# Kernel optimization log

Hardware: AMD Instinct MI355X
Metric: run time of the kernel (lower is better)

## Reference

```python
import jax, jax.numpy as jnp
import numpy as np

N_NODES, N_EDGES = 20000, 400000
IN_DIM, HC, OUT_DIM, EDGE_DIM = 128, 128, 128, 2


def _add_self_loops(src, dst, ea, n):
    # PyG fill_value='mean': self-loop edge_attr = mean of incoming edge_attr
    deg = jax.ops.segment_sum(jnp.ones(src.shape[0], ea.dtype), dst, num_segments=n)
    mean_ea = jax.ops.segment_sum(ea, dst, num_segments=n) / jnp.clip(deg, 1.0)[:, None]
    loop = jnp.arange(n, dtype=src.dtype)
    return (jnp.concatenate([src, loop]), jnp.concatenate([dst, loop]),
            jnp.concatenate([ea, mean_ea], axis=0))


def _gat(x, src, dst, ea, W, att_s, att_d, We, att_e, b, heads, out_ch, concat):
    n = x.shape[0]
    xh = (x @ W).reshape(n, heads, out_ch)                      # [N,H,C]
    a_src = jnp.einsum('nhc,hc->nh', xh, att_s)                  # [N,H]
    a_dst = jnp.einsum('nhc,hc->nh', xh, att_d)
    eh = (ea @ We).reshape(-1, heads, out_ch)                    # [E,H,C]
    a_e = jnp.einsum('ehc,hc->eh', eh, att_e)                    # [E,H]
    alpha = jax.nn.leaky_relu(a_src[src] + a_dst[dst] + a_e, 0.2)
    # segment softmax over destination nodes (every node has a self loop)
    amax = jax.ops.segment_max(alpha, dst, num_segments=n)
    amax = jnp.where(jnp.isfinite(amax), amax, 0.0)
    ex = jnp.exp(alpha - amax[dst])
    denom = jax.ops.segment_sum(ex, dst, num_segments=n)
    w = ex / (denom[dst] + 1e-16)                                # [E,H]
    out = jax.ops.segment_sum(xh[src] * w[..., None], dst, num_segments=n)  # [N,H,C]
    out = out.reshape(n, heads * out_ch) if concat else out.mean(axis=1)
    return out + b


def setup_inputs() -> dict:
    key = jax.random.key(0)
    ks = jax.random.split(key, 16)
    g = lambda k, shape, fan: jax.random.normal(k, shape, jnp.float32) * (1.0 / np.sqrt(fan))
    inp = {
        'x': jax.random.normal(ks[0], (N_NODES, IN_DIM), jnp.float32),
        'edge_index': jax.random.randint(ks[1], (2, N_EDGES), 0, N_NODES, jnp.int32),
        'edge_attr': jax.random.normal(ks[2], (N_EDGES, EDGE_DIM), jnp.float32),
        # conv1: GATConv(128 -> hc=128, heads=2, edge_dim=2, concat=True)
        'W1': g(ks[3], (IN_DIM, 2 * HC), IN_DIM),
        'att_s1': g(ks[4], (2, HC), HC),
        'att_d1': g(ks[5], (2, HC), HC),
        'We1': g(ks[6], (EDGE_DIM, 2 * HC), EDGE_DIM),
        'att_e1': g(ks[7], (2, HC), HC),
        'b1': jnp.zeros((2 * HC,), jnp.float32),
        # conv2: GATConv(256 -> 128, heads=1, edge_dim=2, concat=False)
        'W2': g(ks[8], (2 * HC, OUT_DIM), 2 * HC),
        'att_s2': g(ks[9], (1, OUT_DIM), OUT_DIM),
        'att_d2': g(ks[10], (1, OUT_DIM), OUT_DIM),
        'We2': g(ks[11], (EDGE_DIM, OUT_DIM), EDGE_DIM),
        'att_e2': g(ks[12], (1, OUT_DIM), OUT_DIM),
        'b2': jnp.zeros((OUT_DIM,), jnp.float32),
    }
    return inp


def reference(x, edge_index, edge_attr, W1, att_s1, att_d1, We1, att_e1, b1,
              W2, att_s2, att_d2, We2, att_e2, b2):
    n = x.shape[0]
    src0, dst0 = edge_index[0], edge_index[1]
    src, dst, ea = _add_self_loops(src0, dst0, edge_attr, n)
    x0 = x
    h = jax.nn.relu(_gat(x, src, dst, ea, W1, att_s1, att_d1, We1, att_e1, b1,
                         heads=2, out_ch=HC, concat=True))
    h = _gat(h, src, dst, ea, W2, att_s2, att_d2, We2, att_e2, b2,
             heads=1, out_ch=OUT_DIM, concat=False)
    # SimpleConv(aggr='mean'): mean over incoming neighbors on the ORIGINAL edges
    deg = jax.ops.segment_sum(jnp.ones(src0.shape[0], h.dtype), dst0, num_segments=n)
    mean_h = jax.ops.segment_sum(h[src0], dst0, num_segments=n) / jnp.clip(deg, 1.0)[:, None]
    return jax.nn.relu(mean_h + x0)
```

## Files before the change

kernel.cpp:

```cpp
#include <hip/hip_runtime.h>
#include <hip/hip_bf16.h>

#define NN 20000
#define NE 400000
#define SLOTS 64

typedef unsigned short u16;
typedef unsigned int u32;
typedef unsigned long long u64;

typedef __attribute__((ext_vector_type(8))) short bf16x8;
typedef __attribute__((ext_vector_type(4))) float f32x4;

__device__ __forceinline__ float bf2f(u16 u) {
    union { u32 i; float f; } v; v.i = ((u32)u) << 16; return v.f;
}
__device__ __forceinline__ u16 f2bf(float f) {
    __hip_bfloat16 h = __float2bfloat16(f);
    return *reinterpret_cast<u16*>(&h);
}
__device__ __forceinline__ u32 pack2(float lo, float hi) {
    return (u32)f2bf(lo) | ((u32)f2bf(hi) << 16);
}

__global__ void k_pre(const float* __restrict__ We1, const float* __restrict__ att_e1,
                      const float* __restrict__ We2, const float* __restrict__ att_e2,
                      const float* __restrict__ W1, const float* __restrict__ W2,
                      int* __restrict__ cnt, float* __restrict__ consts,
                      u16* __restrict__ Bt1, u16* __restrict__ Bt2) {
    int idx = blockIdx.x * 256 + threadIdx.x;
    if (idx < NN) cnt[idx] = 0;
    if (idx < 32768) {
        int n = idx >> 7, k = idx & 127;
        Bt1[idx] = f2bf(W1[k * 256 + n]);
    } else {
        int j = idx - 32768;
        int n = j >> 8, k = j & 255;
        Bt2[j] = f2bf(W2[k * 128 + n]);
    }
    if (blockIdx.x == 0) {
        __shared__ float red[128];
        int c = threadIdx.x;
        float p[6];
        if (c < 128) {
            p[0] = We1[0 * 256 + 0 * 128 + c] * att_e1[0 * 128 + c];
            p[1] = We1[0 * 256 + 1 * 128 + c] * att_e1[1 * 128 + c];
            p[2] = We1[1 * 256 + 0 * 128 + c] * att_e1[0 * 128 + c];
            p[3] = We1[1 * 256 + 1 * 128 + c] * att_e1[1 * 128 + c];
            p[4] = We2[0 * 128 + c] * att_e2[c];
            p[5] = We2[1 * 128 + c] * att_e2[c];
        }
        for (int j = 0; j < 6; j++) {
            if (c < 128) red[c] = p[j];
            __syncthreads();
            for (int off = 64; off >= 1; off >>= 1) {
                if (c < off) red[c] += red[c + off];
                __syncthreads();
            }
            if (c == 0) consts[j] = red[0];
            __syncthreads();
        }
    }
}

__global__ void k_build(const int* __restrict__ ei, const float* __restrict__ ea,
                        const float* __restrict__ consts, int* __restrict__ cnt,
                        float4* __restrict__ slot) {
    int e = blockIdx.x * 256 + threadIdx.x;
    if (e >= NE) return;
    int d = ei[NE + e];
    int s = ei[e];
    float2 v = *reinterpret_cast<const float2*>(ea + (size_t)e * 2);
    int pos = atomicAdd(&cnt[d], 1);
    if (pos < SLOTS) {
        float4 rec;
        rec.x = __int_as_float(s);
        rec.y = v.x * consts[0] + v.y * consts[2];
        rec.z = v.x * consts[1] + v.y * consts[3];
        rec.w = v.x * consts[4] + v.y * consts[5];
        slot[d * SLOTS + pos] = rec;
    }
}

__global__ __launch_bounds__(256) void k_gemm1(const float* __restrict__ A,
                                               const u16* __restrict__ Bt,
                                               const float* __restrict__ att_s,
                                               const float* __restrict__ att_d,
                                               u16* __restrict__ C,
                                               float2* __restrict__ a_s,
                                               float2* __restrict__ a_d) {
    constexpr int K = 128, KC = 4, NT = 16;
    int lane = threadIdx.x & 63;
    int wave = threadIdx.x >> 6;
    int r0 = (blockIdx.x * 4 + wave) * 16;
    if (r0 >= NN) return;
    int mrow = lane & 15, g = lane >> 4;
    int arow = r0 + mrow; if (arow >= NN) arow = NN - 1;
    const float* abase = A + (size_t)arow * K + g * 8;
    bf16x8 a[KC];
#pragma unroll
    for (int kc = 0; kc < KC; kc++) {
        float4 lo = *reinterpret_cast<const float4*>(abase + kc * 32);
        float4 hi = *reinterpret_cast<const float4*>(abase + kc * 32 + 4);
        bf16x8 t;
        t[0] = (short)f2bf(lo.x); t[1] = (short)f2bf(lo.y);
        t[2] = (short)f2bf(lo.z); t[3] = (short)f2bf(lo.w);
        t[4] = (short)f2bf(hi.x); t[5] = (short)f2bf(hi.y);
        t[6] = (short)f2bf(hi.z); t[7] = (short)f2bf(hi.w);
        a[kc] = t;
    }
    f32x4 acc[NT];
#pragma unroll
    for (int nt = 0; nt < NT; nt++) acc[nt] = (f32x4){0.f, 0.f, 0.f, 0.f};
#pragma unroll
    for (int nt = 0; nt < NT; nt++) {
        const u16* bbase = Bt + (size_t)(nt * 16 + mrow) * K + g * 8;
#pragma unroll
        for (int kc = 0; kc < KC; kc++) {
            bf16x8 b = *reinterpret_cast<const bf16x8*>(bbase + kc * 32);
            acc[nt] = __builtin_amdgcn_mfma_f32_16x16x32_bf16(a[kc], b, acc[nt], 0, 0, 0);
        }
    }
    int orow0 = r0 + g * 4;
#pragma unroll
    for (int nt = 0; nt < NT; nt++)
#pragma unroll
        for (int r = 0; r < 4; r++) {
            int rr = orow0 + r;
            if (rr < NN) C[(size_t)rr * 256 + nt * 16 + mrow] = f2bf(acc[nt][r]);
        }
    float attsv[NT], attdv[NT];
#pragma unroll
    for (int nt = 0; nt < NT; nt++) {
        attsv[nt] = att_s[nt * 16 + mrow];
        attdv[nt] = att_d[nt * 16 + mrow];
    }
#pragma unroll
    for (int r = 0; r < 4; r++) {
        float s0 = 0.f, s1 = 0.f, d0 = 0.f, d1 = 0.f;
#pragma unroll
        for (int nt = 0; nt < 8; nt++) { s0 += acc[nt][r] * attsv[nt]; d0 += acc[nt][r] * attdv[nt]; }
#pragma unroll
        for (int nt = 8; nt < NT; nt++) { s1 += acc[nt][r] * attsv[nt]; d1 += acc[nt][r] * attdv[nt]; }
        for (int off = 8; off >= 1; off >>= 1) {
            s0 += __shfl_xor(s0, off); s1 += __shfl_xor(s1, off);
            d0 += __shfl_xor(d0, off); d1 += __shfl_xor(d1, off);
        }
        int rr = orow0 + r;
        if (mrow == 0 && rr < NN) {
            a_s[rr] = make_float2(s0, s1);
            a_d[rr] = make_float2(d0, d1);
        }
    }
}

__global__ __launch_bounds__(256) void k_gemm2(const u16* __restrict__ A,
                                               const u16* __restrict__ Bt,
                                               const float* __restrict__ att_s,
                                               const float* __restrict__ att_d,
                                               u16* __restrict__ C,
                                               float* __restrict__ a_s,
                                               float* __restrict__ a_d) {
    constexpr int K = 256, KC = 8, NT = 8;
    int lane = threadIdx.x & 63;
    int wave = threadIdx.x >> 6;
    int r0 = (blockIdx.x * 4 + wave) * 16;
    if (r0 >= NN) return;
    int mrow = lane & 15, g = lane >> 4;
    int arow = r0 + mrow; if (arow >= NN) arow = NN - 1;
    const u16* abase = A + (size_t)arow * K + g * 8;
    bf16x8 a[KC];
#pragma unroll
    for (int kc = 0; kc < KC; kc++) a[kc] = *reinterpret_cast<const bf16x8*>(abase + kc * 32);
    f32x4 acc[NT];
#pragma unroll
    for (int nt = 0; nt < NT; nt++) acc[nt] = (f32x4){0.f, 0.f, 0.f, 0.f};
#pragma unroll
    for (int nt = 0; nt < NT; nt++) {
        const u16* bbase = Bt + (size_t)(nt * 16 + mrow) * K + g * 8;
#pragma unroll
        for (int kc = 0; kc < KC; kc++) {
            bf16x8 b = *reinterpret_cast<const bf16x8*>(bbase + kc * 32);
            acc[nt] = __builtin_amdgcn_mfma_f32_16x16x32_bf16(a[kc], b, acc[nt], 0, 0, 0);
        }
    }
    int orow0 = r0 + g * 4;
#pragma unroll
    for (int nt = 0; nt < NT; nt++)
#pragma unroll
        for (int r = 0; r < 4; r++) {
            int rr = orow0 + r;
            if (rr < NN) C[(size_t)rr * 128 + nt * 16 + mrow] = f2bf(acc[nt][r]);
        }
    float attsv[NT], attdv[NT];
#pragma unroll
    for (int nt = 0; nt < NT; nt++) {
        attsv[nt] = att_s[nt * 16 + mrow];
        attdv[nt] = att_d[nt * 16 + mrow];
    }
#pragma unroll
    for (int r = 0; r < 4; r++) {
        float s0 = 0.f, d0 = 0.f;
#pragma unroll
        for (int nt = 0; nt < NT; nt++) { s0 += acc[nt][r] * attsv[nt]; d0 += acc[nt][r] * attdv[nt]; }
        for (int off = 8; off >= 1; off >>= 1) {
            s0 += __shfl_xor(s0, off);
            d0 += __shfl_xor(d0, off);
        }
        int rr = orow0 + r;
        if (mrow == 0 && rr < NN) { a_s[rr] = s0; a_d[rr] = d0; }
    }
}

__global__ __launch_bounds__(256) void k_conv1(const int* __restrict__ cnt,
                                               const float4* __restrict__ slot,
                                               const u16* __restrict__ xh1,
                                               const float2* __restrict__ a_s,
                                               const float2* __restrict__ a_d,
                                               const float* __restrict__ b1,
                                               u16* __restrict__ h1out) {
    int lane = threadIdx.x & 63;
    int n = blockIdx.x * 4 + (threadIdx.x >> 6);
    if (n >= NN) return;
    int deg = cnt[n]; if (deg > SLOTS) deg = SLOTS;
    float2 ad = a_d[n];
    float2 asn = a_s[n];
    bool valid = lane < deg;
    int s = 0; float ae0 = 0.f, ae1 = 0.f;
    if (valid) {
        float4 rec = slot[n * SLOTS + lane];
        s = __float_as_int(rec.x);
        ae0 = rec.y; ae1 = rec.z;
    }
    float sum0 = ae0, sum1 = ae1;
    for (int off = 32; off >= 1; off >>= 1) {
        sum0 += __shfl_xor(sum0, off);
        sum1 += __shfl_xor(sum1, off);
    }
    float invdeg = 1.f / (float)(deg < 1 ? 1 : deg);
    float sae0 = sum0 * invdeg, sae1 = sum1 * invdeg;
    float2 asv = valid ? a_s[s] : make_float2(0.f, 0.f);
    float l0 = asv.x + ad.x + ae0;
    float l1 = asv.y + ad.y + ae1;
    l0 = l0 >= 0.f ? l0 : 0.2f * l0;
    l1 = l1 >= 0.f ? l1 : 0.2f * l1;
    if (!valid) { l0 = -3.4e38f; l1 = -3.4e38f; }
    float sl0 = asn.x + ad.x + sae0;
    float sl1 = asn.y + ad.y + sae1;
    sl0 = sl0 >= 0.f ? sl0 : 0.2f * sl0;
    sl1 = sl1 >= 0.f ? sl1 : 0.2f * sl1;
    float cm0 = l0, cm1 = l1;
    for (int off = 32; off >= 1; off >>= 1) {
        cm0 = fmaxf(cm0, __shfl_xor(cm0, off));
        cm1 = fmaxf(cm1, __shfl_xor(cm1, off));
    }
    float m0 = fmaxf(cm0, sl0), m1 = fmaxf(cm1, sl1);
    float e0 = valid ? __expf(l0 - m0) : 0.f;
    float e1 = valid ? __expf(l1 - m1) : 0.f;
    float es0 = __expf(sl0 - m0), es1 = __expf(sl1 - m1);
    float cs0 = e0, cs1 = e1;
    for (int off = 32; off >= 1; off >>= 1) {
        cs0 += __shfl_xor(cs0, off);
        cs1 += __shfl_xor(cs1, off);
    }
    float den0 = cs0 + es0 + 1e-16f, den1 = cs1 + es1 + 1e-16f;
    int q = lane >> 4, ql = lane & 15;
    int ch = ql * 16;
    int myh = ql >> 3;
    float acc[16];
#pragma unroll
    for (int i = 0; i < 16; i++) acc[i] = 0.f;
    for (int j = 0; j < deg; j += 4) {
        int jj = j + q;
        bool ve = jj < deg;
        int sj = ve ? __shfl(s, jj) : n;
        float w0 = __shfl(e0, jj), w1 = __shfl(e1, jj);
        float wj = ve ? (myh ? w1 : w0) : 0.f;
        const u16* p = xh1 + (size_t)sj * 256 + ch;
        uint4 va = *reinterpret_cast<const uint4*>(p);
        uint4 vb = *reinterpret_cast<const uint4*>(p + 8);
        acc[0] += wj * bf2f((u16)(va.x & 0xffff)); acc[1] += wj * bf2f((u16)(va.x >> 16));
        acc[2] += wj * bf2f((u16)(va.y & 0xffff)); acc[3] += wj * bf2f((u16)(va.y >> 16));
        acc[4] += wj * bf2f((u16)(va.z & 0xffff)); acc[5] += wj * bf2f((u16)(va.z >> 16));
        acc[6] += wj * bf2f((u16)(va.w & 0xffff)); acc[7] += wj * bf2f((u16)(va.w >> 16));
        acc[8] += wj * bf2f((u16)(vb.x & 0xffff)); acc[9] += wj * bf2f((u16)(vb.x >> 16));
        acc[10] += wj * bf2f((u16)(vb.y & 0xffff)); acc[11] += wj * bf2f((u16)(vb.y >> 16));
        acc[12] += wj * bf2f((u16)(vb.z & 0xffff)); acc[13] += wj * bf2f((u16)(vb.z >> 16));
        acc[14] += wj * bf2f((u16)(vb.w & 0xffff)); acc[15] += wj * bf2f((u16)(vb.w >> 16));
    }
#pragma unroll
    for (int i = 0; i < 16; i++) {
        acc[i] += __shfl_xor(acc[i], 16);
        acc[i] += __shfl_xor(acc[i], 32);
    }
    if (q == 0) {
        float ws = myh ? es1 : es0;
        const u16* p = xh1 + (size_t)n * 256 + ch;
        uint4 va = *reinterpret_cast<const uint4*>(p);
        uint4 vb = *reinterpret_cast<const uint4*>(p + 8);
        acc[0] += ws * bf2f((u16)(va.x & 0xffff)); acc[1] += ws * bf2f((u16)(va.x >> 16));
        acc[2] += ws * bf2f((u16)(va.y & 0xffff)); acc[3] += ws * bf2f((u16)(va.y >> 16));
        acc[4] += ws * bf2f((u16)(va.z & 0xffff)); acc[5] += ws * bf2f((u16)(va.z >> 16));
        acc[6] += ws * bf2f((u16)(va.w & 0xffff)); acc[7] += ws * bf2f((u16)(va.w >> 16));
        acc[8] += ws * bf2f((u16)(vb.x & 0xffff)); acc[9] += ws * bf2f((u16)(vb.x >> 16));
        acc[10] += ws * bf2f((u16)(vb.y & 0xffff)); acc[11] += ws * bf2f((u16)(vb.y >> 16));
        acc[12] += ws * bf2f((u16)(vb.z & 0xffff)); acc[13] += ws * bf2f((u16)(vb.z >> 16));
        acc[14] += ws * bf2f((u16)(vb.w & 0xffff)); acc[15] += ws * bf2f((u16)(vb.w >> 16));
        float inv = 1.f / (myh ? den1 : den0);
        float o[16];
#pragma unroll
        for (int i = 0; i < 4; i++) {
            float4 b4 = *reinterpret_cast<const float4*>(b1 + ch + i * 4);
            o[i * 4 + 0] = acc[i * 4 + 0] * inv + b4.x;
            o[i * 4 + 1] = acc[i * 4 + 1] * inv + b4.y;
            o[i * 4 + 2] = acc[i * 4 + 2] * inv + b4.z;
            o[i * 4 + 3] = acc[i * 4 + 3] * inv + b4.w;
        }
#pragma unroll
        for (int i = 0; i < 16; i++) o[i] = o[i] > 0.f ? o[i] : 0.f;
        uint4 sa, sb;
        sa.x = pack2(o[0], o[1]);  sa.y = pack2(o[2], o[3]);
        sa.z = pack2(o[4], o[5]);  sa.w = pack2(o[6], o[7]);
        sb.x = pack2(o[8], o[9]);  sb.y = pack2(o[10], o[11]);
        sb.z = pack2(o[12], o[13]); sb.w = pack2(o[14], o[15]);
        *reinterpret_cast<uint4*>(h1out + (size_t)n * 256 + ch) = sa;
        *reinterpret_cast<uint4*>(h1out + (size_t)n * 256 + ch + 8) = sb;
    }
}

__global__ __launch_bounds__(256) void k_conv2(const int* __restrict__ cnt,
                                               const float4* __restrict__ slot,
                                               const u16* __restrict__ xh2,
                                               const float* __restrict__ a_s,
                                               const float* __restrict__ a_d,
                                               const float* __restrict__ b2v,
                                               u16* __restrict__ h2out) {
    int lane = threadIdx.x & 63;
    int n = blockIdx.x * 4 + (threadIdx.x >> 6);
    if (n >= NN) return;
    int deg = cnt[n]; if (deg > SLOTS) deg = SLOTS;
    float ad = a_d[n];
    float asn = a_s[n];
    bool valid = lane < deg;
    int s = 0; float ae = 0.f;
    if (valid) {
        float4 rec = slot[n * SLOTS + lane];
        s = __float_as_int(rec.x);
        ae = rec.w;
    }
    float sum = ae;
    for (int off = 32; off >= 1; off >>= 1) sum += __shfl_xor(sum, off);
    float invdeg = 1.f / (float)(deg < 1 ? 1 : deg);
    float sae = sum * invdeg;
    float l = (valid ? a_s[s] : 0.f) + ad + ae;
    l = l >= 0.f ? l : 0.2f * l;
    if (!valid) l = -3.4e38f;
    float sl = asn + ad + sae;
    sl = sl >= 0.f ? sl : 0.2f * sl;
    float cm = l;
    for (int off = 32; off >= 1; off >>= 1) cm = fmaxf(cm, __shfl_xor(cm, off));
    float m = fmaxf(cm, sl);
    float e = valid ? __expf(l - m) : 0.f;
    float es = __expf(sl - m);
    float cs = e;
    for (int off = 32; off >= 1; off >>= 1) cs += __shfl_xor(cs, off);
    float den = cs + es + 1e-16f;
    int q = lane >> 4, ql = lane & 15;
    int ch = ql * 8;
    float acc[8];
#pragma unroll
    for (int i = 0; i < 8; i++) acc[i] = 0.f;
    for (int j = 0; j < deg; j += 4) {
        int jj = j + q;
        bool ve = jj < deg;
        int sj = ve ? __shfl(s, jj) : n;
        float wj = ve ? __shfl(e, jj) : 0.f;
        uint4 v = *reinterpret_cast<const uint4*>(xh2 + (size_t)sj * 128 + ch);
        acc[0] += wj * bf2f((u16)(v.x & 0xffff)); acc[1] += wj * bf2f((u16)(v.x >> 16));
        acc[2] += wj * bf2f((u16)(v.y & 0xffff)); acc[3] += wj * bf2f((u16)(v.y >> 16));
        acc[4] += wj * bf2f((u16)(v.z & 0xffff)); acc[5] += wj * bf2f((u16)(v.z >> 16));
        acc[6] += wj * bf2f((u16)(v.w & 0xffff)); acc[7] += wj * bf2f((u16)(v.w >> 16));
    }
#pragma unroll
    for (int i = 0; i < 8; i++) {
        acc[i] += __shfl_xor(acc[i], 16);
        acc[i] += __shfl_xor(acc[i], 32);
    }
    if (q == 0) {
        uint4 v = *reinterpret_cast<const uint4*>(xh2 + (size_t)n * 128 + ch);
        acc[0] += es * bf2f((u16)(v.x & 0xffff)); acc[1] += es * bf2f((u16)(v.x >> 16));
        acc[2] += es * bf2f((u16)(v.y & 0xffff)); acc[3] += es * bf2f((u16)(v.y >> 16));
        acc[4] += es * bf2f((u16)(v.z & 0xffff)); acc[5] += es * bf2f((u16)(v.z >> 16));
        acc[6] += es * bf2f((u16)(v.w & 0xffff)); acc[7] += es * bf2f((u16)(v.w >> 16));
        float inv = 1.f / den;
        float4 ba = *reinterpret_cast<const float4*>(b2v + ch);
        float4 bb = *reinterpret_cast<const float4*>(b2v + ch + 4);
        uint4 st;
        st.x = pack2(acc[0] * inv + ba.x, acc[1] * inv + ba.y);
        st.y = pack2(acc[2] * inv + ba.z, acc[3] * inv + ba.w);
        st.z = pack2(acc[4] * inv + bb.x, acc[5] * inv + bb.y);
        st.w = pack2(acc[6] * inv + bb.z, acc[7] * inv + bb.w);
        *reinterpret_cast<uint4*>(h2out + (size_t)n * 128 + ch) = st;
    }
}

__global__ __launch_bounds__(256) void k_final(const int* __restrict__ cnt,
                                               const float4* __restrict__ slot,
                                               const u16* __restrict__ h2,
                                               const float* __restrict__ x,
                                               float* __restrict__ out) {
    int lane = threadIdx.x & 63;
    int n = blockIdx.x * 4 + (threadIdx.x >> 6);
    if (n >= NN) return;
    int deg = cnt[n]; if (deg > SLOTS) deg = SLOTS;
    int s = (lane < deg) ? __float_as_int(slot[n * SLOTS + lane].x) : 0;
    int q = lane >> 4, ql = lane & 15;
    int ch = ql * 8;
    float acc[8];
#pragma unroll
    for (int i = 0; i < 8; i++) acc[i] = 0.f;
    for (int j = 0; j < deg; j += 4) {
        int jj = j + q;
        bool ve = jj < deg;
        int sj = ve ? __shfl(s, jj) : n;
        float wj = ve ? 1.f : 0.f;
        uint4 v = *reinterpret_cast<const uint4*>(h2 + (size_t)sj * 128 + ch);
        acc[0] += wj * bf2f((u16)(v.x & 0xffff)); acc[1] += wj * bf2f((u16)(v.x >> 16));
        acc[2] += wj * bf2f((u16)(v.y & 0xffff)); acc[3] += wj * bf2f((u16)(v.y >> 16));
        acc[4] += wj * bf2f((u16)(v.z & 0xffff)); acc[5] += wj * bf2f((u16)(v.z >> 16));
        acc[6] += wj * bf2f((u16)(v.w & 0xffff)); acc[7] += wj * bf2f((u16)(v.w >> 16));
    }
#pragma unroll
    for (int i = 0; i < 8; i++) {
        acc[i] += __shfl_xor(acc[i], 16);
        acc[i] += __shfl_xor(acc[i], 32);
    }
    if (q == 0) {
        float invd = 1.f / (float)(deg < 1 ? 1 : deg);
        float4 xa = *reinterpret_cast<const float4*>(x + (size_t)n * 128 + ch);
        float4 xb = *reinterpret_cast<const float4*>(x + (size_t)n * 128 + ch + 4);
        float o0 = acc[0] * invd + xa.x, o1 = acc[1] * invd + xa.y;
        float o2 = acc[2] * invd + xa.z, o3 = acc[3] * invd + xa.w;
        float o4 = acc[4] * invd + xb.x, o5 = acc[5] * invd + xb.y;
        float o6 = acc[6] * invd + xb.z, o7 = acc[7] * invd + xb.w;
        float4 sa = make_float4(o0 > 0.f ? o0 : 0.f, o1 > 0.f ? o1 : 0.f,
                                o2 > 0.f ? o2 : 0.f, o3 > 0.f ? o3 : 0.f);
        float4 sb = make_float4(o4 > 0.f ? o4 : 0.f, o5 > 0.f ? o5 : 0.f,
                                o6 > 0.f ? o6 : 0.f, o7 > 0.f ? o7 : 0.f);
        *reinterpret_cast<float4*>(out + (size_t)n * 128 + ch) = sa;
        *reinterpret_cast<float4*>(out + (size_t)n * 128 + ch + 4) = sb;
    }
}

extern "C" void kernel_launch(void* const* d_in, const int* in_sizes, int n_in,
                              void* d_out, int out_size, void* d_ws, size_t ws_size,
                              hipStream_t stream) {
    const float* x      = (const float*)d_in[0];
    const int*   ei     = (const int*)d_in[1];
    const float* ea     = (const float*)d_in[2];
    const float* W1     = (const float*)d_in[3];
    const float* att_s1 = (const float*)d_in[4];
    const float* att_d1 = (const float*)d_in[5];
    const float* We1    = (const float*)d_in[6];
    const float* att_e1 = (const float*)d_in[7];
    const float* b1     = (const float*)d_in[8];
    const float* W2     = (const float*)d_in[9];
    const float* att_s2 = (const float*)d_in[10];
    const float* att_d2 = (const float*)d_in[11];
    const float* We2    = (const float*)d_in[12];
    const float* att_e2 = (const float*)d_in[13];
    const float* b2     = (const float*)d_in[14];
    float* out = (float*)d_out;

    char* w = (char*)d_ws;
    auto alloc = [&](size_t bytes) -> void* {
        void* p = (void*)w;
        w += (bytes + 255) & ~(size_t)255;
        return p;
    };
    int*    cnt    = (int*)alloc(NN * 4);
    float*  consts = (float*)alloc(64);
    float4* slot   = (float4*)alloc((size_t)NN * SLOTS * 16);
    u16*    Bt1    = (u16*)alloc(256 * 128 * 2);
    u16*    Bt2    = (u16*)alloc(128 * 256 * 2);
    u16*    xh1b   = (u16*)alloc((size_t)NN * 256 * 2);
    u16*    h1b    = (u16*)alloc((size_t)NN * 256 * 2);
    float2* a_s1   = (float2*)alloc(NN * 8);
    float2* a_d1   = (float2*)alloc(NN * 8);
    float*  a_s2   = (float*)alloc(NN * 4);
    float*  a_d2   = (float*)alloc(NN * 4);
    u16* xh2b = xh1b;
    u16* h2b  = h1b;

    k_pre<<<256, 256, 0, stream>>>(We1, att_e1, We2, att_e2, W1, W2, cnt, consts, Bt1, Bt2);
    k_build<<<(NE + 255) / 256, 256, 0, stream>>>(ei, ea, consts, cnt, slot);

    k_gemm1<<<(NN + 63) / 64, 256, 0, stream>>>(x, Bt1, att_s1, att_d1, xh1b, a_s1, a_d1);
    k_conv1<<<(NN + 3) / 4, 256, 0, stream>>>(cnt, slot, xh1b, a_s1, a_d1, b1, h1b);
    k_gemm2<<<(NN + 63) / 64, 256, 0, stream>>>(h1b, Bt2, att_s2, att_d2, xh2b, a_s2, a_d2);
    k_conv2<<<(NN + 3) / 4, 256, 0, stream>>>(cnt, slot, xh2b, a_s2, a_d2, b2, h2b);
    k_final<<<(NN + 3) / 4, 256, 0, stream>>>(cnt, slot, h2b, x, out);
}
```

Baseline: 142.9 us.

## Compact edge slot records to 8 bytes and widen gather to 8 edges per wave

Result: slower. 146.5 us (+2.5%).

```diff
diff --git a/kernel.cpp b/kernel.cpp
--- a/kernel.cpp
+++ b/kernel.cpp
@@ -64,22 +64,14 @@
 }
 
 __global__ void k_build(const int* __restrict__ ei, const float* __restrict__ ea,
-                        const float* __restrict__ consts, int* __restrict__ cnt,
-                        float4* __restrict__ slot) {
+                        int* __restrict__ cnt, uint2* __restrict__ slot) {
     int e = blockIdx.x * 256 + threadIdx.x;
     if (e >= NE) return;
     int d = ei[NE + e];
     int s = ei[e];
     float2 v = *reinterpret_cast<const float2*>(ea + (size_t)e * 2);
     int pos = atomicAdd(&cnt[d], 1);
-    if (pos < SLOTS) {
-        float4 rec;
-        rec.x = __int_as_float(s);
-        rec.y = v.x * consts[0] + v.y * consts[2];
-        rec.z = v.x * consts[1] + v.y * consts[3];
-        rec.w = v.x * consts[4] + v.y * consts[5];
-        slot[d * SLOTS + pos] = rec;
-    }
+    if (pos < SLOTS) slot[d * SLOTS + pos] = make_uint2((u32)s, pack2(v.x, v.y));
 }
 
 __global__ __launch_bounds__(256) void k_gemm1(const float* __restrict__ A,
@@ -213,7 +205,8 @@
 }
 
 __global__ __launch_bounds__(256) void k_conv1(const int* __restrict__ cnt,
-                                               const float4* __restrict__ slot,
+                                               const uint2* __restrict__ slot,
+                                               const float* __restrict__ consts,
                                                const u16* __restrict__ xh1,
                                                const float2* __restrict__ a_s,
                                                const float2* __restrict__ a_d,
@@ -223,14 +216,18 @@
     int n = blockIdx.x * 4 + (threadIdx.x >> 6);
     if (n >= NN) return;
     int deg = cnt[n]; if (deg > SLOTS) deg = SLOTS;
+    float c00 = consts[0], c01 = consts[1], c10 = consts[2], c11 = consts[3];
     float2 ad = a_d[n];
     float2 asn = a_s[n];
     bool valid = lane < deg;
     int s = 0; float ae0 = 0.f, ae1 = 0.f;
     if (valid) {
-        float4 rec = slot[n * SLOTS + lane];
-        s = __float_as_int(rec.x);
-        ae0 = rec.y; ae1 = rec.z;
+        uint2 rec = slot[n * SLOTS + lane];
+        s = (int)rec.x;
+        float e0v = bf2f((u16)(rec.y & 0xffff));
+        float e1v = bf2f((u16)(rec.y >> 16));
+        ae0 = e0v * c00 + e1v * c10;
+        ae1 = e0v * c01 + e1v * c11;
     }
     float sum0 = ae0, sum1 = ae1;
     for (int off = 32; off >= 1; off >>= 1) {
@@ -329,7 +326,8 @@
 }
 
 __global__ __launch_bounds__(256) void k_conv2(const int* __restrict__ cnt,
-                                               const float4* __restrict__ slot,
+                                               const uint2* __restrict__ slot,
+                                               const float* __restrict__ consts,
                                                const u16* __restrict__ xh2,
                                                const float* __restrict__ a_s,
                                                const float* __restrict__ a_d,
@@ -339,14 +337,15 @@
     int n = blockIdx.x * 4 + (threadIdx.x >> 6);
     if (n >= NN) return;
     int deg = cnt[n]; if (deg > SLOTS) deg = SLOTS;
+    float d0c = consts[4], d1c = consts[5];
     float ad = a_d[n];
     float asn = a_s[n];
     bool valid = lane < deg;
     int s = 0; float ae = 0.f;
     if (valid) {
-        float4 rec = slot[n * SLOTS + lane];
-        s = __float_as_int(rec.x);
-        ae = rec.w;
+        uint2 rec = slot[n * SLOTS + lane];
+        s = (int)rec.x;
+        ae = bf2f((u16)(rec.y & 0xffff)) * d0c + bf2f((u16)(rec.y >> 16)) * d1c;
     }
     float sum = ae;
     for (int off = 32; off >= 1; off >>= 1) sum += __shfl_xor(sum, off);
@@ -365,47 +364,68 @@
     float cs = e;
     for (int off = 32; off >= 1; off >>= 1) cs += __shfl_xor(cs, off);
     float den = cs + es + 1e-16f;
-    int q = lane >> 4, ql = lane & 15;
-    int ch = ql * 8;
-    float acc[8];
-#pragma unroll
-    for (int i = 0; i < 8; i++) acc[i] = 0.f;
-    for (int j = 0; j < deg; j += 4) {
-        int jj = j + q;
+    int g = lane >> 3, gl = lane & 7;
+    int ch = gl * 16;
+    float acc[16];
+#pragma unroll
+    for (int i = 0; i < 16; i++) acc[i] = 0.f;
+    for (int j = 0; j < deg; j += 8) {
+        int jj = j + g;
         bool ve = jj < deg;
         int sj = ve ? __shfl(s, jj) : n;
         float wj = ve ? __shfl(e, jj) : 0.f;
-        uint4 v = *reinterpret_cast<const uint4*>(xh2 + (size_t)sj * 128 + ch);
-        acc[0] += wj * bf2f((u16)(v.x & 0xffff)); acc[1] += wj * bf2f((u16)(v.x >> 16));
-        acc[2] += wj * bf2f((u16)(v.y & 0xffff)); acc[3] += wj * bf2f((u16)(v.y >> 16));
-        acc[4] += wj * bf2f((u16)(v.z & 0xffff)); acc[5] += wj * bf2f((u16)(v.z >> 16));
-        acc[6] += wj * bf2f((u16)(v.w & 0xffff)); acc[7] += wj * bf2f((u16)(v.w >> 16));
-    }
-#pragma unroll
-    for (int i = 0; i < 8; i++) {
+        const u16* p = xh2 + (size_t)sj * 128 + ch;
+        uint4 va = *reinterpret_cast<const uint4*>(p);
+        uint4 vb = *reinterpret_cast<const uint4*>(p + 8);
+        acc[0] += wj * bf2f((u16)(va.x & 0xffff)); acc[1] += wj * bf2f((u16)(va.x >> 16));
+        acc[2] += wj * bf2f((u16)(va.y & 0xffff)); acc[3] += wj * bf2f((u16)(va.y >> 16));
+        acc[4] += wj * bf2f((u16)(va.z & 0xffff)); acc[5] += wj * bf2f((u16)(va.z >> 16));
+        acc[6] += wj * bf2f((u16)(va.w & 0xffff)); acc[7] += wj * bf2f((u16)(va.w >> 16));
+        acc[8] += wj * bf2f((u16)(vb.x & 0xffff)); acc[9] += wj * bf2f((u16)(vb.x >> 16));
+        acc[10] += wj * bf2f((u16)(vb.y & 0xffff)); acc[11] += wj * bf2f((u16)(vb.y >> 16));
+        acc[12] += wj * bf2f((u16)(vb.z & 0xffff)); acc[13] += wj * bf2f((u16)(vb.z >> 16));
+        acc[14] += wj * bf2f((u16)(vb.w & 0xffff)); acc[15] += wj * bf2f((u16)(vb.w >> 16));
+    }
+#pragma unroll
+    for (int i = 0; i < 16; i++) {
+        acc[i] += __shfl_xor(acc[i], 8);
         acc[i] += __shfl_xor(acc[i], 16);
         acc[i] += __shfl_xor(acc[i], 32);
     }
-    if (q == 0) {
-        uint4 v = *reinterpret_cast<const uint4*>(xh2 + (size_t)n * 128 + ch);
-        acc[0] += es * bf2f((u16)(v.x & 0xffff)); acc[1] += es * bf2f((u16)(v.x >> 16));
-        acc[2] += es * bf2f((u16)(v.y & 0xffff)); acc[3] += es * bf2f((u16)(v.y >> 16));
-        acc[4] += es * bf2f((u16)(v.z & 0xffff)); acc[5] += es * bf2f((u16)(v.z >> 16));
-        acc[6] += es * bf2f((u16)(v.w & 0xffff)); acc[7] += es * bf2f((u16)(v.w >> 16));
+    if (lane < 8) {
+        const u16* p = xh2 + (size_t)n * 128 + ch;
+        uint4 va = *reinterpret_cast<const uint4*>(p);
+        uint4 vb = *reinterpret_cast<const uint4*>(p + 8);
+        acc[0] += es * bf2f((u16)(va.x & 0xffff)); acc[1] += es * bf2f((u16)(va.x >> 16));
+        acc[2] += es * bf2f((u16)(va.y & 0xffff)); acc[3] += es * bf2f((u16)(va.y >> 16));
+        acc[4] += es * bf2f((u16)(va.z & 0xffff)); acc[5] += es * bf2f((u16)(va.z >> 16));
+        acc[6] += es * bf2f((u16)(va.w & 0xffff)); acc[7] += es * bf2f((u16)(va.w >> 16));
+        acc[8] += es * bf2f((u16)(vb.x & 0xffff)); acc[9] += es * bf2f((u16)(vb.x >> 16));
+        acc[10] += es * bf2f((u16)(vb.y & 0xffff)); acc[11] += es * bf2f((u16)(vb.y >> 16));
+        acc[12] += es * bf2f((u16)(vb.z & 0xffff)); acc[13] += es * bf2f((u16)(vb.z >> 16));
+        acc[14] += es * bf2f((u16)(vb.w & 0xffff)); acc[15] += es * bf2f((u16)(vb.w >> 16));
         float inv = 1.f / den;
-        float4 ba = *reinterpret_cast<const float4*>(b2v + ch);
-        float4 bb = *reinterpret_cast<const float4*>(b2v + ch + 4);
-        uint4 st;
-        st.x = pack2(acc[0] * inv + ba.x, acc[1] * inv + ba.y);
-        st.y = pack2(acc[2] * inv + ba.z, acc[3] * inv + ba.w);
-        st.z = pack2(acc[4] * inv + bb.x, acc[5] * inv + bb.y);
-        st.w = pack2(acc[6] * inv + bb.z, acc[7] * inv + bb.w);
-        *reinterpret_cast<uint4*>(h2out + (size_t)n * 128 + ch) = st;
+        float o[16];
+#pragma unroll
+        for (int i = 0; i < 4; i++) {
+            float4 b4 = *reinterpret_cast<const float4*>(b2v + ch + i * 4);
+            o[i * 4 + 0] = acc[i * 4 + 0] * inv + b4.x;
+            o[i * 4 + 1] = acc[i * 4 + 1] * inv + b4.y;
+            o[i * 4 + 2] = acc[i * 4 + 2] * inv + b4.z;
+            o[i * 4 + 3] = acc[i * 4 + 3] * inv + b4.w;
+        }
+        uint4 sa, sb;
+        sa.x = pack2(o[0], o[1]);  sa.y = pack2(o[2], o[3]);
+        sa.z = pack2(o[4], o[5]);  sa.w = pack2(o[6], o[7]);
+        sb.x = pack2(o[8], o[9]);  sb.y = pack2(o[10], o[11]);
+        sb.z = pack2(o[12], o[13]); sb.w = pack2(o[14], o[15]);
+        *reinterpret_cast<uint4*>(h2out + (size_t)n * 128 + ch) = sa;
+        *reinterpret_cast<uint4*>(h2out + (size_t)n * 128 + ch + 8) = sb;
     }
 }
 
 __global__ __launch_bounds__(256) void k_final(const int* __restrict__ cnt,
-                                               const float4* __restrict__ slot,
+                                               const uint2* __restrict__ slot,
                                                const u16* __restrict__ h2,
                                                const float* __restrict__ x,
                                                float* __restrict__ out) {
@@ -413,42 +433,54 @@
     int n = blockIdx.x * 4 + (threadIdx.x >> 6);
     if (n >= NN) return;
     int deg = cnt[n]; if (deg > SLOTS) deg = SLOTS;
-    int s = (lane < deg) ? __float_as_int(slot[n * SLOTS + lane].x) : 0;
-    int q = lane >> 4, ql = lane & 15;
-    int ch = ql * 8;
-    float acc[8];
-#pragma unroll
-    for (int i = 0; i < 8; i++) acc[i] = 0.f;
-    for (int j = 0; j < deg; j += 4) {
-        int jj = j + q;
+    int s = (lane < deg) ? (int)slot[n * SLOTS + lane].x : 0;
+    int g = lane >> 3, gl = lane & 7;
+    int ch = gl * 16;
+    float acc[16];
+#pragma unroll
+    for (int i = 0; i < 16; i++) acc[i] = 0.f;
+    for (int j = 0; j < deg; j += 8) {
+        int jj = j + g;
         bool ve = jj < deg;
         int sj = ve ? __shfl(s, jj) : n;
         float wj = ve ? 1.f : 0.f;
-        uint4 v = *reinterpret_cast<const uint4*>(h2 + (size_t)sj * 128 + ch);
-        acc[0] += wj * bf2f((u16)(v.x & 0xffff)); acc[1] += wj * bf2f((u16)(v.x >> 16));
-        acc[2] += wj * bf2f((u16)(v.y & 0xffff)); acc[3] += wj * bf2f((u16)(v.y >> 16));
-        acc[4] += wj * bf2f((u16)(v.z & 0xffff)); acc[5] += wj * bf2f((u16)(v.z >> 16));
-        acc[6] += wj * bf2f((u16)(v.w & 0xffff)); acc[7] += wj * bf2f((u16)(v.w >> 16));
-    }
-#pragma unroll
-    for (int i = 0; i < 8; i++) {
+        const u16* p = h2 + (size_t)sj * 128 + ch;
+        uint4 va = *reinterpret_cast<const uint4*>(p);
+        uint4 vb = *reinterpret_cast<const uint4*>(p + 8);
+        acc[0] += wj * bf2f((u16)(va.x & 0xffff)); acc[1] += wj * bf2f((u16)(va.x >> 16));
+        acc[2] += wj * bf2f((u16)(va.y & 0xffff)); acc[3] += wj * bf2f((u16)(va.y >> 16));
+        acc[4] += wj * bf2f((u16)(va.z & 0xffff)); acc[5] += wj * bf2f((u16)(va.z >> 16));
+        acc[6] += wj * bf2f((u16)(va.w & 0xffff)); acc[7] += wj * bf2f((u16)(va.w >> 16));
+        acc[8] += wj * bf2f((u16)(vb.x & 0xffff)); acc[9] += wj * bf2f((u16)(vb.x >> 16));
+        acc[10] += wj * bf2f((u16)(vb.y & 0xffff)); acc[11] += wj * bf2f((u16)(vb.y >> 16));
+        acc[12] += wj * bf2f((u16)(vb.z & 0xffff)); acc[13] += wj * bf2f((u16)(vb.z >> 16));
+        acc[14] += wj * bf2f((u16)(vb.w & 0xffff)); acc[15] += wj * bf2f((u16)(vb.w >> 16));
+    }
+#pragma unroll
+    for (int i = 0; i < 16; i++) {
+        acc[i] += __shfl_xor(acc[i], 8);
         acc[i] += __shfl_xor(acc[i], 16);
         acc[i] += __shfl_xor(acc[i], 32);
     }
-    if (q == 0) {
+    if (lane < 8) {
         float invd = 1.f / (float)(deg < 1 ? 1 : deg);
-        float4 xa = *reinterpret_cast<const float4*>(x + (size_t)n * 128 + ch);
-        float4 xb = *reinterpret_cast<const float4*>(x + (size_t)n * 128 + ch + 4);
-        float o0 = acc[0] * invd + xa.x, o1 = acc[1] * invd + xa.y;
-        float o2 = acc[2] * invd + xa.z, o3 = acc[3] * invd + xa.w;
-        float o4 = acc[4] * invd + xb.x, o5 = acc[5] * invd + xb.y;
-        float o6 = acc[6] * invd + xb.z, o7 = acc[7] * invd + xb.w;
-        float4 sa = make_float4(o0 > 0.f ? o0 : 0.f, o1 > 0.f ? o1 : 0.f,
-                                o2 > 0.f ? o2 : 0.f, o3 > 0.f ? o3 : 0.f);
-        float4 sb = make_float4(o4 > 0.f ? o4 : 0.f, o5 > 0.f ? o5 : 0.f,
-                                o6 > 0.f ? o6 : 0.f, o7 > 0.f ? o7 : 0.f);
-        *reinterpret_cast<float4*>(out + (size_t)n * 128 + ch) = sa;
-        *reinterpret_cast<float4*>(out + (size_t)n * 128 + ch + 4) = sb;
+        float o[16];
+#pragma unroll
+        for (int i = 0; i < 4; i++) {
+            float4 xa = *reinterpret_cast<const float4*>(x + (size_t)n * 128 + ch + i * 4);
+            o[i * 4 + 0] = acc[i * 4 + 0] * invd + xa.x;
+            o[i * 4 + 1] = acc[i * 4 + 1] * invd + xa.y;
+            o[i * 4 + 2] = acc[i * 4 + 2] * invd + xa.z;
+            o[i * 4 + 3] = acc[i * 4 + 3] * invd + xa.w;
+        }
+#pragma unroll
+        for (int i = 0; i < 4; i++) {
+            float4 st = make_float4(o[i*4+0] > 0.f ? o[i*4+0] : 0.f,
+                                    o[i*4+1] > 0.f ? o[i*4+1] : 0.f,
+                                    o[i*4+2] > 0.f ? o[i*4+2] : 0.f,
+                                    o[i*4+3] > 0.f ? o[i*4+3] : 0.f);
+            *reinterpret_cast<float4*>(out + (size_t)n * 128 + ch + i * 4) = st;
+        }
     }
 }
 
@@ -480,7 +512,7 @@
     };
     int*    cnt    = (int*)alloc(NN * 4);
     float*  consts = (float*)alloc(64);
-    float4* slot   = (float4*)alloc((size_t)NN * SLOTS * 16);
+    uint2*  slot   = (uint2*)alloc((size_t)NN * SLOTS * 8);
     u16*    Bt1    = (u16*)alloc(256 * 128 * 2);
     u16*    Bt2    = (u16*)alloc(128 * 256 * 2);
     u16*    xh1b   = (u16*)alloc((size_t)NN * 256 * 2);
@@ -493,11 +525,11 @@
     u16* h2b  = h1b;
 
     k_pre<<<256, 256, 0, stream>>>(We1, att_e1, We2, att_e2, W1, W2, cnt, consts, Bt1, Bt2);
-    k_build<<<(NE + 255) / 256, 256, 0, stream>>>(ei, ea, consts, cnt, slot);
+    k_build<<<(NE + 255) / 256, 256, 0, stream>>>(ei, ea, cnt, slot);
 
     k_gemm1<<<(NN + 63) / 64, 256, 0, stream>>>(x, Bt1, att_s1, att_d1, xh1b, a_s1, a_d1);
-    k_conv1<<<(NN + 3) / 4, 256, 0, stream>>>(cnt, slot, xh1b, a_s1, a_d1, b1, h1b);
+    k_conv1<<<(NN + 3) / 4, 256, 0, stream>>>(cnt, slot, consts, xh1b, a_s1, a_d1, b1, h1b);
     k_gemm2<<<(NN + 63) / 64, 256, 0, stream>>>(h1b, Bt2, att_s2, att_d2, xh2b, a_s2, a_d2);
-    k_conv2<<<(NN + 3) / 4, 256, 0, stream>>>(cnt, slot, xh2b, a_s2, a_d2, b2, h2b);
+    k_conv2<<<(NN + 3) / 4, 256, 0, stream>>>(cnt, slot, consts, xh2b, a_s2, a_d2, b2, h2b);
     k_final<<<(NN + 3) / 4, 256, 0, stream>>>(cnt, slot, h2b, x, out);
 }
```

## Merge edge-build into GEMM1 launch and compress slot records to fp16 edge attrs

Applied to the files above, without the earlier changes.

Measured after the change: 145.4 us. Within noise of the previous version (+1.7%).

```diff
diff --git a/kernel.cpp b/kernel.cpp
--- a/kernel.cpp
+++ b/kernel.cpp
@@ -1,9 +1,11 @@
 #include <hip/hip_runtime.h>
 #include <hip/hip_bf16.h>
+#include <hip/hip_fp16.h>
 
 #define NN 20000
 #define NE 400000
 #define SLOTS 64
+#define NBUILD 1563
 
 typedef unsigned short u16;
 typedef unsigned int u32;
@@ -21,6 +23,14 @@
 }
 __device__ __forceinline__ u32 pack2(float lo, float hi) {
     return (u32)f2bf(lo) | ((u32)f2bf(hi) << 16);
+}
+__device__ __forceinline__ u16 f2h(float f) {
+    __half h = __float2half(f);
+    return *reinterpret_cast<u16*>(&h);
+}
+__device__ __forceinline__ float h2f(u16 u) {
+    __half h = *reinterpret_cast<__half*>(&u);
+    return __half2float(h);
 }
 
 __global__ void k_pre(const float* __restrict__ We1, const float* __restrict__ att_e1,
@@ -63,36 +73,36 @@
     }
 }
 
-__global__ void k_build(const int* __restrict__ ei, const float* __restrict__ ea,
-                        const float* __restrict__ consts, int* __restrict__ cnt,
-                        float4* __restrict__ slot) {
-    int e = blockIdx.x * 256 + threadIdx.x;
-    if (e >= NE) return;
-    int d = ei[NE + e];
-    int s = ei[e];
-    float2 v = *reinterpret_cast<const float2*>(ea + (size_t)e * 2);
-    int pos = atomicAdd(&cnt[d], 1);
-    if (pos < SLOTS) {
-        float4 rec;
-        rec.x = __int_as_float(s);
-        rec.y = v.x * consts[0] + v.y * consts[2];
-        rec.z = v.x * consts[1] + v.y * consts[3];
-        rec.w = v.x * consts[4] + v.y * consts[5];
-        slot[d * SLOTS + pos] = rec;
-    }
-}
-
-__global__ __launch_bounds__(256) void k_gemm1(const float* __restrict__ A,
-                                               const u16* __restrict__ Bt,
-                                               const float* __restrict__ att_s,
-                                               const float* __restrict__ att_d,
-                                               u16* __restrict__ C,
-                                               float2* __restrict__ a_s,
-                                               float2* __restrict__ a_d) {
+__global__ __launch_bounds__(256) void k_fat1(const int* __restrict__ ei,
+                                              const float* __restrict__ ea,
+                                              int* __restrict__ cnt,
+                                              uint2* __restrict__ slot,
+                                              const float* __restrict__ A,
+                                              const u16* __restrict__ Bt,
+                                              const float* __restrict__ att_s,
+                                              const float* __restrict__ att_d,
+                                              u16* __restrict__ C,
+                                              float2* __restrict__ a_s,
+                                              float2* __restrict__ a_d) {
+    if (blockIdx.x < NBUILD) {
+        int e = blockIdx.x * 256 + threadIdx.x;
+        if (e < NE) {
+            int d = ei[NE + e];
+            int s = ei[e];
+            float2 v = *reinterpret_cast<const float2*>(ea + (size_t)e * 2);
+            int pos = atomicAdd(&cnt[d], 1);
+            if (pos < SLOTS) {
+                u32 eh = (u32)f2h(v.x) | ((u32)f2h(v.y) << 16);
+                slot[d * SLOTS + pos] = make_uint2((u32)s, eh);
+            }
+        }
+        return;
+    }
     constexpr int K = 128, KC = 4, NT = 16;
+    int gb = blockIdx.x - NBUILD;
     int lane = threadIdx.x & 63;
     int wave = threadIdx.x >> 6;
-    int r0 = (blockIdx.x * 4 + wave) * 16;
+    int r0 = (gb * 4 + wave) * 16;
     if (r0 >= NN) return;
     int mrow = lane & 15, g = lane >> 4;
     int arow = r0 + mrow; if (arow >= NN) arow = NN - 1;
@@ -213,7 +223,8 @@
 }
 
 __global__ __launch_bounds__(256) void k_conv1(const int* __restrict__ cnt,
-                                               const float4* __restrict__ slot,
+                                               const uint2* __restrict__ slot,
+                                               const float* __restrict__ consts,
                                                const u16* __restrict__ xh1,
                                                const float2* __restrict__ a_s,
                                                const float2* __restrict__ a_d,
@@ -223,14 +234,18 @@
     int n = blockIdx.x * 4 + (threadIdx.x >> 6);
     if (n >= NN) return;
     int deg = cnt[n]; if (deg > SLOTS) deg = SLOTS;
+    float c00 = consts[0], c01 = consts[1], c10 = consts[2], c11 = consts[3];
     float2 ad = a_d[n];
     float2 asn = a_s[n];
     bool valid = lane < deg;
     int s = 0; float ae0 = 0.f, ae1 = 0.f;
     if (valid) {
-        float4 rec = slot[n * SLOTS + lane];
-        s = __float_as_int(rec.x);
-        ae0 = rec.y; ae1 = rec.z;
+        uint2 rec = slot[n * SLOTS + lane];
+        s = (int)rec.x;
+        float e0v = h2f((u16)(rec.y & 0xffff));
+        float e1v = h2f((u16)(rec.y >> 16));
+        ae0 = e0v * c00 + e1v * c10;
+        ae1 = e0v * c01 + e1v * c11;
     }
     float sum0 = ae0, sum1 = ae1;
     for (int off = 32; off >= 1; off >>= 1) {
@@ -329,7 +344,8 @@
 }
 
 __global__ __launch_bounds__(256) void k_conv2(const int* __restrict__ cnt,
-                                               const float4* __restrict__ slot,
+                                               const uint2* __restrict__ slot,
+                                               const float* __restrict__ consts,
                                                const u16* __restrict__ xh2,
                                                const float* __restrict__ a_s,
                                                const float* __restrict__ a_d,
@@ -339,14 +355,15 @@
     int n = blockIdx.x * 4 + (threadIdx.x >> 6);
     if (n >= NN) return;
     int deg = cnt[n]; if (deg > SLOTS) deg = SLOTS;
+    float d0c = consts[4], d1c = consts[5];
     float ad = a_d[n];
     float asn = a_s[n];
     bool valid = lane < deg;
     int s = 0; float ae = 0.f;
     if (valid) {
-        float4 rec = slot[n * SLOTS + lane];
-        s = __float_as_int(rec.x);
-        ae = rec.w;
+        uint2 rec = slot[n * SLOTS + lane];
+        s = (int)rec.x;
+        ae = h2f((u16)(rec.y & 0xffff)) * d0c + h2f((u16)(rec.y >> 16)) * d1c;
     }
     float sum = ae;
     for (int off = 32; off >= 1; off >>= 1) sum += __shfl_xor(sum, off);
@@ -405,7 +422,7 @@
 }
 
 __global__ __launch_bounds__(256) void k_final(const int* __restrict__ cnt,
-                                               const float4* __restrict__ slot,
+                                               const uint2* __restrict__ slot,
                                                const u16* __restrict__ h2,
                                                const float* __restrict__ x,
                                                float* __restrict__ out) {
@@ -413,7 +430,7 @@
     int n = blockIdx.x * 4 + (threadIdx.x >> 6);
     if (n >= NN) return;
     int deg = cnt[n]; if (deg > SLOTS) deg = SLOTS;
-    int s = (lane < deg) ? __float_as_int(slot[n * SLOTS + lane].x) : 0;
+    int s = (lane < deg) ? (int)slot[n * SLOTS + lane].x : 0;
     int q = lane >> 4, ql = lane & 15;
     int ch = ql * 8;
     float acc[8];
@@ -480,7 +497,7 @@
     };
     int*    cnt    = (int*)alloc(NN * 4);
     float*  consts = (float*)alloc(64);
-    float4* slot   = (float4*)alloc((size_t)NN * SLOTS * 16);
+    uint2*  slot   = (uint2*)alloc((size_t)NN * SLOTS * 8);
     u16*    Bt1    = (u16*)alloc(256 * 128 * 2);
     u16*    Bt2    = (u16*)alloc(128 * 256 * 2);
     u16*    xh1b   = (u16*)alloc((size_t)NN * 256 * 2);
@@ -493,11 +510,11 @@
     u16* h2b  = h1b;
 
     k_pre<<<256, 256, 0, stream>>>(We1, att_e1, We2, att_e2, W1, W2, cnt, consts, Bt1, Bt2);
-    k_build<<<(NE + 255) / 256, 256, 0, stream>>>(ei, ea, consts, cnt, slot);
-
-    k_gemm1<<<(NN + 63) / 64, 256, 0, stream>>>(x, Bt1, att_s1, att_d1, xh1b, a_s1, a_d1);
-    k_conv1<<<(NN + 3) / 4, 256, 0, stream>>>(cnt, slot, xh1b, a_s1, a_d1, b1, h1b);
+    k_fat1<<<NBUILD + (NN + 63) / 64, 256, 0, stream>>>(ei, ea, cnt, slot,
+                                                        x, Bt1, att_s1, att_d1,
+                                                        xh1b, a_s1, a_d1);
+    k_conv1<<<(NN + 3) / 4, 256, 0, stream>>>(cnt, slot, consts, xh1b, a_s1, a_d1, b1, h1b);
     k_gemm2<<<(NN + 63) / 64, 256, 0, stream>>>(h1b, Bt2, att_s2, att_d2, xh2b, a_s2, a_d2);
-    k_conv2<<<(NN + 3) / 4, 256, 0, stream>>>(cnt, slot, xh2b, a_s2, a_d2, b2, h2b);
+    k_conv2<<<(NN + 3) / 4, 256, 0, stream>>>(cnt, slot, consts, xh2b, a_s2, a_d2, b2, h2b);
     k_final<<<(NN + 3) / 4, 256, 0, stream>>>(cnt, slot, h2b, x, out);
 }
```
